# Performance work log

Measured on AMD Instinct MI355X. Metric: run time of the kernel, lower is better.

Reference implementation:

```python
import jax, jax.numpy as jnp
import numpy as np

N_NODES = 100000
N_EDGES = 1600000
D_IN = 128
D_HID = 128
D_OUT = 64


def setup_inputs() -> dict:
    key = jax.random.key(0)
    ks = jax.random.split(key, 8)
    x = jax.random.normal(ks[0], (N_NODES, D_IN), dtype=jnp.float32)
    edge_index = jax.random.randint(ks[1], (2, N_EDGES), 0, N_NODES, dtype=jnp.int64)
    s = 1.0 / np.sqrt(D_IN)
    W1l = jax.random.uniform(ks[2], (D_IN, D_HID), minval=-s, maxval=s, dtype=jnp.float32)
    W1r = jax.random.uniform(ks[3], (D_IN, D_HID), minval=-s, maxval=s, dtype=jnp.float32)
    b1 = jnp.zeros((D_HID,), dtype=jnp.float32)
    s2 = 1.0 / np.sqrt(D_HID)
    W2l = jax.random.uniform(ks[4], (D_HID, D_OUT), minval=-s2, maxval=s2, dtype=jnp.float32)
    W2r = jax.random.uniform(ks[5], (D_HID, D_OUT), minval=-s2, maxval=s2, dtype=jnp.float32)
    b2 = jnp.zeros((D_OUT,), dtype=jnp.float32)
    return {"x": x, "edge_index": edge_index, "drpt": 0,
            "W1l": W1l, "W1r": W1r, "b1": b1,
            "W2l": W2l, "W2r": W2r, "b2": b2}


def _mean_aggregate(x, src, dst, n_nodes):
    # gather source features along edges, scatter-mean to destinations
    gathered = x[src]                                   # [E, d]
    summed = jax.ops.segment_sum(gathered, dst, num_segments=n_nodes)  # [N, d]
    deg = jax.ops.segment_sum(jnp.ones((src.shape[0],), x.dtype), dst,
                              num_segments=n_nodes)     # [N]
    return summed / jnp.maximum(deg, 1.0)[:, None]


def _sage_conv(x, src, dst, Wl, Wr, b):
    # PyG SAGEConv (mean): out = agg @ Wl + b + x @ Wr
    agg = _mean_aggregate(x, src, dst, x.shape[0])
    return agg @ Wl + b + x @ Wr


def reference(x, edge_index, drpt, W1l, W1r, b1, W2l, W2r, b2):
    src, dst = edge_index[0], edge_index[1]
    h = _sage_conv(x, src, dst, W1l, W1r, b1)
    h = jax.nn.relu(h)
    # dropout is identity at inference (training=False)
    out = _sage_conv(h, src, dst, W2l, W2r, b2)
    return out
```

## Files before the change

kernel.cpp:

```cpp
#include <hip/hip_runtime.h>
#include <hip/hip_bf16.h>


#define N_NODES 100000
#define NGRP 6250
#define NBKT 391
#define ECHUNK 8192
#define BCAP 12288
#define NXB 12500
#define NWB 192

typedef __attribute__((ext_vector_type(8))) short short8v;
typedef __attribute__((ext_vector_type(4))) float f32x4;
typedef __attribute__((ext_vector_type(2))) uint u32x2;

__device__ inline ushort bf16_rne(float f) {
    union { float f; uint u; } c; c.f = f;
    uint u = c.u;
    return (ushort)((u + 0x7FFFu + ((u >> 16) & 1u)) >> 16);
}
__device__ inline float bf16_f(ushort h) {
    union { uint u; float f; } c; c.u = (uint)h << 16;
    return c.f;
}
__device__ inline unsigned char fp8_enc(float f) {
    union { float f; uint u; } c; c.f = f;
    uint u = c.u;
    uint s = (u >> 24) & 0x80u;
    uint a = u & 0x7FFFFFFFu;
    uint code;
    if (a >= 0x3C800000u) {
        uint r = a + 0x7FFFFu + ((a >> 20) & 1u);
        int e = (int)(r >> 23) - 120;
        uint mm = (r >> 20) & 7u;
        code = ((uint)e << 3) | mm;
        if (code > 0x7Eu) code = 0x7Eu;
    } else {
        code = (uint)(__uint_as_float(a) * 512.0f + 0.5f);
    }
    return (unsigned char)(s | code);
}

__device__ inline void gl_lds16(const void* g, void* l) {
    __builtin_amdgcn_global_load_lds(
        (const __attribute__((address_space(1))) uint*)g,
        (__attribute__((address_space(3))) uint*)l, 16, 0, 0);
}
__device__ inline uint lds_off(const void* p) {
    return (uint)(size_t)(const __attribute__((address_space(3))) char*)p;
}

__global__ __launch_bounds__(256) void k_prep(const float* __restrict__ x,
                                              const float* __restrict__ W1l,
                                              const float* __restrict__ W1r,
                                              const float* __restrict__ W2l,
                                              const float* __restrict__ W2r,
                                              const int* __restrict__ dst, int E,
                                              ushort* __restrict__ xh,
                                              unsigned char* __restrict__ xf8,
                                              ushort* __restrict__ BT1h,
                                              ushort* __restrict__ BT1l,
                                              ushort* __restrict__ BT2h,
                                              ushort* __restrict__ BT2l,
                                              int* __restrict__ bhist) {
    __shared__ int hsh[NBKT];
    const int b = blockIdx.x;
    if (b < NXB) {
        int i = (b * 256 + threadIdx.x) * 4;
        float4 v = *(const float4*)&x[i];
        ushort4 hh;
        hh.x = bf16_rne(v.x); hh.y = bf16_rne(v.y);
        hh.z = bf16_rne(v.z); hh.w = bf16_rne(v.w);
        *(ushort4*)&xh[i] = hh;
        uint f8 = (uint)fp8_enc(v.x) | ((uint)fp8_enc(v.y) << 8) |
                  ((uint)fp8_enc(v.z) << 16) | ((uint)fp8_enc(v.w) << 24);
        *(uint*)&xf8[i] = f8;
    } else if (b < NXB + NWB) {
        int id = (b - NXB) * 256 + threadIdx.x;
        if (id < 32768) {
            int n = id >> 8, k = id & 255;
            float v = (k < 128) ? W1l[k * 128 + n] : W1r[(k - 128) * 128 + n];
            ushort h = bf16_rne(v);
            BT1h[id] = h;
            BT1l[id] = bf16_rne(v - bf16_f(h));
        } else {
            int i = id - 32768;
            int n = i >> 7, k = i & 127;
            float v = (n < 64) ? W2l[k * 64 + n] : W2r[k * 64 + (n - 64)];
            ushort h = bf16_rne(v);
            BT2h[i] = h;
            BT2l[i] = bf16_rne(v - bf16_f(h));
        }
    } else {
        int bb = b - NXB - NWB;
        for (int i = threadIdx.x; i < NBKT; i += 256) hsh[i] = 0;
        __syncthreads();
        int b0 = bb * ECHUNK;
        for (int i = threadIdx.x; i < ECHUNK; i += 256) {
            int e = b0 + i;
            if (e < E) atomicAdd(&hsh[dst[e] >> 8], 1);
        }
        __syncthreads();
        for (int i = threadIdx.x; i < NBKT; i += 256)
            if (hsh[i]) atomicAdd(&bhist[i], hsh[i]);
    }
}

__global__ __launch_bounds__(512) void kA2_scan(const int* __restrict__ bhist,
                                                int* __restrict__ boff,
                                                int* __restrict__ bcur) {
    __shared__ int s[512];
    int t = threadIdx.x;
    s[t] = (t < NBKT) ? bhist[t] : 0;
    __syncthreads();
    for (int d = 1; d < 512; d <<= 1) {
        int v = (t >= d) ? s[t - d] : 0;
        __syncthreads();
        s[t] += v;
        __syncthreads();
    }
    if (t <= NBKT) {
        int e = (t == 0) ? 0 : s[t - 1];
        boff[t] = e;
        if (t < NBKT) bcur[t] = e;
    }
}

__global__ __launch_bounds__(256) void kA3_scatter(const int* __restrict__ src,
                                                   const int* __restrict__ dst,
                                                   int* __restrict__ bcur,
                                                   int* __restrict__ pairs, int E) {
    __shared__ int hist[NBKT];
    __shared__ int base[NBKT];
    __shared__ ushort rank[ECHUNK];
    for (int i = threadIdx.x; i < NBKT; i += 256) hist[i] = 0;
    __syncthreads();
    int b0 = blockIdx.x * ECHUNK;
    for (int i = threadIdx.x; i < ECHUNK; i += 256) {
        int e = b0 + i;
        if (e < E) rank[i] = (ushort)atomicAdd(&hist[dst[e] >> 8], 1);
    }
    __syncthreads();
    for (int i = threadIdx.x; i < NBKT; i += 256) {
        int c = hist[i];
        base[i] = c ? atomicAdd(&bcur[i], c) : 0;
    }
    __syncthreads();
    for (int i = threadIdx.x; i < ECHUNK; i += 256) {
        int e = b0 + i;
        if (e < E) {
            int d = dst[e];
            pairs[base[d >> 8] + rank[i]] = src[e] | ((d & 255) << 17);
        }
    }
}

__global__ __launch_bounds__(256) void kB_build(const int* __restrict__ pairs,
                                                const int* __restrict__ boff,
                                                int* __restrict__ csr,
                                                unsigned char* __restrict__ ldst,
                                                int* __restrict__ offsets,
                                                float* __restrict__ invdeg,
                                                int N, int E) {
    __shared__ int cnt[256];
    __shared__ int sc[256];
    __shared__ int cur[256];
    __shared__ int stage[BCAP];
    const int b = blockIdx.x;
    const int gbase = boff[b], gcount = boff[b + 1] - gbase;
    const int n0 = b << 8;
    const int t = threadIdx.x;

    cnt[t] = 0;
    __syncthreads();
    for (int i = t; i < gcount; i += 256)
        atomicAdd(&cnt[pairs[gbase + i] >> 17], 1);
    __syncthreads();
    sc[t] = cnt[t];
    __syncthreads();
    for (int d = 1; d < 256; d <<= 1) {
        int v = (t >= d) ? sc[t - d] : 0;
        __syncthreads();
        sc[t] += v;
        __syncthreads();
    }
    int excl = sc[t] - cnt[t];
    cur[t] = excl;
    int node = n0 + t;
    if (node < N) {
        offsets[node] = gbase + excl;
        invdeg[node] = 1.0f / fmaxf((float)cnt[t], 1.0f);
    }
    if (b == NBKT - 1 && t == 0) offsets[N] = E;
    __syncthreads();

    if (gcount <= BCAP) {
        for (int i = t; i < gcount; i += 256) {
            int p = pairs[gbase + i];
            int pos = atomicAdd(&cur[p >> 17], 1);
            stage[pos] = p;
        }
        __syncthreads();
        for (int i = t; i < gcount; i += 256) {
            int p = stage[i];
            csr[gbase + i] = p & 0x1FFFF;
            ldst[gbase + i] = (unsigned char)((p >> 17) & 15);
        }
    } else {
        for (int i = t; i < gcount; i += 256) {
            int p = pairs[gbase + i];
            int pos = atomicAdd(&cur[p >> 17], 1);
            csr[gbase + pos] = p & 0x1FFFF;
            ldst[gbase + pos] = (unsigned char)((p >> 17) & 15);
        }
    }
}

__global__ __launch_bounds__(256) void k_agg1(const unsigned char* __restrict__ xf8,
                                              const int* __restrict__ csr,
                                              const unsigned char* __restrict__ ldst,
                                              const int* __restrict__ off,
                                              const float* __restrict__ invdeg,
                                              ushort* __restrict__ ah, int E) {
    __shared__ char smem[32768];
    const int wv = threadIdx.x >> 6, lane = threadIdx.x & 63;
    const int g = blockIdx.x;
    const int gbase = off[g * 16], gend = off[g * 16 + 16];
    const int cnt = gend - gbase;
    const int m = lane & 15;
    const int e_meta = lane & 31;
    const int t_hi = lane >> 5;
    const int Emax = E - 1;
    char* stg = smem + wv * 4096;

    f32x4 acc[8] = {};
    const int nch = (cnt + 31) >> 5;

    int p0 = gbase + wv * 32;
    int se = csr[(p0 + e_meta < Emax) ? p0 + e_meta : Emax];
    int lb = (p0 + e_meta < gend) ? (int)ldst[p0 + e_meta] : 255;

    for (int ch = wv; ch < nch; ch += 4) {
        const char* rowbase = (const char*)xf8 + (size_t)se * 128;
        #pragma unroll
        for (int c = 0; c < 4; ++c)
            gl_lds16(rowbase + (c * 2 + t_hi) * 16, stg + c * 1024);

        asm volatile("s_waitcnt vmcnt(0)" ::: "memory");
        __builtin_amdgcn_sched_barrier(0);

        unsigned long long av = 0ull;
        #pragma unroll
        for (int j = 0; j < 8; ++j) {
            int k = (lane >> 4) * 8 + j;
            int b = __shfl(lb, k);
            av |= (b == m) ? (0x38ull << (8 * j)) : 0ull;
        }

        u32x2 tb[8];
        uint base0 = lds_off(stg) + lane * 8;
        #pragma unroll
        for (int t = 0; t < 8; ++t) {
            uint a1 = base0 + t * 512;
            asm volatile("ds_read_b64_tr_b8 %0, %1" : "=v"(tb[t]) : "v"(a1));
        }
        asm volatile("s_waitcnt lgkmcnt(0)" ::: "memory");
        __builtin_amdgcn_sched_barrier(0);
        #pragma unroll
        for (int t = 0; t < 8; ++t) {
            unsigned long long bv = ((unsigned long long)tb[t].y << 32) | tb[t].x;
            acc[t] = __builtin_amdgcn_mfma_f32_16x16x32_fp8_fp8(
                (long long)av, (long long)bv, acc[t], 0, 0, 0);
        }

        int p = gbase + (ch + 4) * 32;
        se = csr[(p + e_meta < Emax) ? p + e_meta : Emax];
        lb = (p + e_meta < gend) ? (int)ldst[p + e_meta] : 255;
    }

    __syncthreads();
    f32x4* red = (f32x4*)smem;
    #pragma unroll
    for (int t = 0; t < 8; ++t) red[(wv * 8 + t) * 64 + lane] = acc[t];
    __syncthreads();

    float idv[4];
    #pragma unroll
    for (int i = 0; i < 4; ++i) idv[i] = invdeg[g * 16 + (lane >> 4) * 4 + i];
    #pragma unroll
    for (int tt = 0; tt < 2; ++tt) {
        int t = wv * 2 + tt;
        f32x4 s = red[t * 64 + lane];
        s += red[(8 + t) * 64 + lane];
        s += red[(16 + t) * 64 + lane];
        s += red[(24 + t) * 64 + lane];
        #pragma unroll
        for (int i = 0; i < 4; ++i) {
            int node = g * 16 + (lane >> 4) * 4 + i;
            ah[(size_t)node * 128 + t * 16 + m] = bf16_rne(s[i] * idv[i]);
        }
    }
}

__global__ __launch_bounds__(256) void k_agg2(const ushort* __restrict__ hWl,
                                              const float* __restrict__ hWr,
                                              const int* __restrict__ csr,
                                              const unsigned char* __restrict__ ldst,
                                              const int* __restrict__ off,
                                              const float* __restrict__ invdeg,
                                              const float* __restrict__ b2,
                                              float* __restrict__ out, int E) {
    __shared__ char smem[16384];
    const int wv = threadIdx.x >> 6, lane = threadIdx.x & 63;
    const int g = blockIdx.x;
    const int gbase = off[g * 16], gend = off[g * 16 + 16];
    const int cnt = gend - gbase;
    const int m = lane & 15;
    const int phys = lane >> 3;
    const int E4 = (phys < 4) ? phys * 2 : (phys - 4) * 2 + 1;
    const int e_st = E4 * 4 + ((lane >> 1) & 3);
    const int e_meta = lane & 31;
    const int Emax = E - 1;
    char* stg = smem + wv * 4096;

    f32x4 acc[4] = {};
    const int nch = (cnt + 31) >> 5;

    int p0 = gbase + wv * 32;
    int se = csr[(p0 + e_st < Emax) ? p0 + e_st : Emax];
    int lb = (p0 + e_meta < gend) ? (int)ldst[p0 + e_meta] : 255;

    for (int ch = wv; ch < nch; ch += 4) {
        const char* gsrc = (const char*)hWl + (size_t)se * 128 + (lane & 1) * 16;
        #pragma unroll
        for (int c = 0; c < 4; ++c)
            gl_lds16(gsrc + c * 32, stg + c * 1024);

        asm volatile("s_waitcnt vmcnt(0)" ::: "memory");
        __builtin_amdgcn_sched_barrier(0);

        uint au[4];
        #pragma unroll
        for (int jp = 0; jp < 4; ++jp) {
            int k0 = (lane >> 4) * 8 + jp * 2;
            int b0 = __shfl(lb, k0);
            int b1 = __shfl(lb, k0 + 1);
            au[jp] = ((b0 == m) ? 0x3F80u : 0u) | (((b1 == m) ? 0x3F80u : 0u) << 16);
        }
        union { uint u[4]; short8v v; } A_;
        A_.u[0] = au[0]; A_.u[1] = au[1]; A_.u[2] = au[2]; A_.u[3] = au[3];

        u32x2 t1[4], t2[4];
        uint base0 = lds_off(stg) + lane * 8;
        #pragma unroll
        for (int t = 0; t < 4; ++t) {
            uint a1 = base0 + t * 1024;
            uint a2 = a1 + 512;
            asm volatile("ds_read_b64_tr_b16 %0, %1" : "=v"(t1[t]) : "v"(a1));
            asm volatile("ds_read_b64_tr_b16 %0, %1" : "=v"(t2[t]) : "v"(a2));
        }
        asm volatile("s_waitcnt lgkmcnt(0)" ::: "memory");
        __builtin_amdgcn_sched_barrier(0);
        #pragma unroll
        for (int t = 0; t < 4; ++t) {
            union { uint u[4]; short8v v; } B_;
            B_.u[0] = t1[t].x; B_.u[1] = t1[t].y;
            B_.u[2] = t2[t].x; B_.u[3] = t2[t].y;
            acc[t] = __builtin_amdgcn_mfma_f32_16x16x32_bf16(A_.v, B_.v, acc[t], 0, 0, 0);
        }

        int p = gbase + (ch + 4) * 32;
        se = csr[(p + e_st < Emax) ? p + e_st : Emax];
        lb = (p + e_meta < gend) ? (int)ldst[p + e_meta] : 255;
    }

    __syncthreads();
    f32x4* red = (f32x4*)smem;
    #pragma unroll
    for (int t = 0; t < 4; ++t) red[(wv * 4 + t) * 64 + lane] = acc[t];
    __syncthreads();

    float idv[4];
    #pragma unroll
    for (int i = 0; i < 4; ++i) idv[i] = invdeg[g * 16 + (lane >> 4) * 4 + i];
    {
        int t = wv;
        f32x4 s = red[t * 64 + lane];
        s += red[(4 + t) * 64 + lane];
        s += red[(8 + t) * 64 + lane];
        s += red[(12 + t) * 64 + lane];
        #pragma unroll
        for (int i = 0; i < 4; ++i) {
            int node = g * 16 + (lane >> 4) * 4 + i;
            size_t idx = (size_t)node * 64 + t * 16 + m;
            out[idx] = s[i] * idv[i] + hWr[idx] + b2[t * 16 + m];
        }
    }
}

__global__ __launch_bounds__(256) void k_mfma12(
    const ushort* __restrict__ Agg, const ushort* __restrict__ X,
    const ushort* __restrict__ B1h, const ushort* __restrict__ B1l,
    const ushort* __restrict__ B2h, const ushort* __restrict__ B2l,
    const float* __restrict__ b1,
    ushort* __restrict__ hWl, float* __restrict__ hWr, int M) {
    __shared__ ushort Ah[128 * 40], Bh[128 * 40], Bl[128 * 40];
    __shared__ ushort hT[4 * 128 * 40];

    const int tid = threadIdx.x;
    const int wid = tid >> 6, lane = tid & 63;
    const int wm = wid >> 1, wn = wid & 1;
    const int m0 = blockIdx.x * 128;
    const int rl = lane & 15, kof = (lane >> 4) * 8;
    const int rq = lane >> 4;

    f32x4 acc[4][4] = {};
    for (int kc = 0; kc < 8; ++kc) {
        #pragma unroll
        for (int r = 0; r < 2; ++r) {
            int chunk = tid + 256 * r;
            int row = chunk >> 2, cq = chunk & 3;
            int gk = kc * 32 + cq * 8;
            int ldso = row * 40 + cq * 8;
            int grow = m0 + row;
            if (grow >= M) grow = M - 1;
            if (gk >= 128) {
                *(short8v*)&Ah[ldso] = *(const short8v*)&X[(size_t)grow * 128 + gk - 128];
            } else {
                *(short8v*)&Ah[ldso] = *(const short8v*)&Agg[(size_t)grow * 128 + gk];
            }
            *(short8v*)&Bh[ldso] = *(const short8v*)&B1h[row * 256 + gk];
            *(short8v*)&Bl[ldso] = *(const short8v*)&B1l[row * 256 + gk];
        }
        __syncthreads();

        short8v a_h[4], b_h[4], b_l[4];
        #pragma unroll
        for (int f = 0; f < 4; ++f) {
            int ra = wm * 64 + f * 16 + rl;
            int rb = wn * 64 + f * 16 + rl;
            a_h[f] = *(const short8v*)&Ah[ra * 40 + kof];
            b_h[f] = *(const short8v*)&Bh[rb * 40 + kof];
            b_l[f] = *(const short8v*)&Bl[rb * 40 + kof];
        }
        #pragma unroll
        for (int mf = 0; mf < 4; ++mf)
            #pragma unroll
            for (int nf = 0; nf < 4; ++nf) {
                acc[mf][nf] = __builtin_amdgcn_mfma_f32_16x16x32_bf16(a_h[mf], b_h[nf], acc[mf][nf], 0, 0, 0);
                acc[mf][nf] = __builtin_amdgcn_mfma_f32_16x16x32_bf16(a_h[mf], b_l[nf], acc[mf][nf], 0, 0, 0);
            }
        __syncthreads();
    }

    #pragma unroll
    for (int mf = 0; mf < 4; ++mf)
        #pragma unroll
        for (int nf = 0; nf < 4; ++nf) {
            int col = wn * 64 + nf * 16 + rl;
            float bv = b1[col];
            #pragma unroll
            for (int i = 0; i < 4; ++i) {
                int rloc = wm * 64 + mf * 16 + rq * 4 + i;
                float v = fmaxf(acc[mf][nf][i] + bv, 0.0f);
                hT[((col >> 5) * 128 + rloc) * 40 + (col & 31)] = bf16_rne(v);
            }
        }
    __syncthreads();

    f32x4 acc2[4][4] = {};
    for (int kc = 0; kc < 4; ++kc) {
        #pragma unroll
        for (int r = 0; r < 2; ++r) {
            int chunk = tid + 256 * r;
            int row = chunk >> 2, cq = chunk & 3;
            int gk = kc * 32 + cq * 8;
            int ldso = row * 40 + cq * 8;
            *(short8v*)&Bh[ldso] = *(const short8v*)&B2h[row * 128 + gk];
            *(short8v*)&Bl[ldso] = *(const short8v*)&B2l[row * 128 + gk];
        }
        __syncthreads();

        short8v a_h[4], b_h[4], b_l[4];
        #pragma unroll
        for (int f = 0; f < 4; ++f) {
            int ra = wm * 64 + f * 16 + rl;
            int rb = wn * 64 + f * 16 + rl;
            a_h[f] = *(const short8v*)&hT[(kc * 128 + ra) * 40 + kof];
            b_h[f] = *(const short8v*)&Bh[rb * 40 + kof];
            b_l[f] = *(const short8v*)&Bl[rb * 40 + kof];
        }
        #pragma unroll
        for (int mf = 0; mf < 4; ++mf)
            #pragma unroll
            for (int nf = 0; nf < 4; ++nf) {
                acc2[mf][nf] = __builtin_amdgcn_mfma_f32_16x16x32_bf16(a_h[mf], b_h[nf], acc2[mf][nf], 0, 0, 0);
                acc2[mf][nf] = __builtin_amdgcn_mfma_f32_16x16x32_bf16(a_h[mf], b_l[nf], acc2[mf][nf], 0, 0, 0);
            }
        __syncthreads();
    }

    #pragma unroll
    for (int mf = 0; mf < 4; ++mf)
        #pragma unroll
        for (int nf = 0; nf < 4; ++nf) {
            int col = wn * 64 + nf * 16 + rl;
            #pragma unroll
            for (int i = 0; i < 4; ++i) {
                int row = m0 + wm * 64 + mf * 16 + rq * 4 + i;
                if (row < M) {
                    float v = acc2[mf][nf][i];
                    if (col < 64) hWl[(size_t)row * 64 + col] = bf16_rne(v);
                    else          hWr[(size_t)row * 64 + col - 64] = v;
                }
            }
        }
}

extern "C" void kernel_launch(void* const* d_in, const int* in_sizes, int n_in,
                              void* d_out, int out_size, void* d_ws, size_t ws_size,
                              hipStream_t stream) {
    const float* x   = (const float*)d_in[0];
    const int*   ei  = (const int*)d_in[1];
    const float* W1l = (const float*)d_in[3];
    const float* W1r = (const float*)d_in[4];
    const float* b1  = (const float*)d_in[5];
    const float* W2l = (const float*)d_in[6];
    const float* W2r = (const float*)d_in[7];
    const float* b2  = (const float*)d_in[8];
    float* out = (float*)d_out;

    const int N = N_NODES;
    const int E = in_sizes[1] / 2;
    const int* src = ei;
    const int* dst = ei + E;
    const int NEB = (E + ECHUNK - 1) / ECHUNK;

    char* ws = (char*)d_ws;
    int*           bhist   = (int*)   (ws + 0);
    int*           boff    = (int*)   (ws + 4096);
    int*           bcur    = (int*)   (ws + 8192);
    int*           offsets = (int*)   (ws + 12288);
    float*         invdeg  = (float*) (ws + 417792);
    int*           csr     = (int*)   (ws + 819200);
    unsigned char* ldst    = (unsigned char*)(ws + 7220224);
    unsigned char* x_f8    = (unsigned char*)(ws + 8821760);
    ushort*        x_hi    = (ushort*)(ws + 21622784);
    ushort*        agg_hi  = (ushort*)(ws + 47223808);
    float*         hWr     = (float*) (ws + 98425856);
    ushort*        BT1h    = (ushort*)(ws + 124026880);
    ushort*        BT1l    = (ushort*)(ws + 124092416);
    ushort*        BT2h    = (ushort*)(ws + 124157952);
    ushort*        BT2l    = (ushort*)(ws + 124190720);
    int*           pairs   = (int*)   (ws + 98425856);
    ushort*        hWl     = (ushort*)(ws + 72824832);

    hipMemsetAsync(bhist, 0, NBKT * 4, stream);

    k_prep<<<NXB + NWB + NEB, 256, 0, stream>>>(x, W1l, W1r, W2l, W2r, dst, E,
                                                x_hi, x_f8, BT1h, BT1l, BT2h, BT2l, bhist);
    kA2_scan<<<1, 512, 0, stream>>>(bhist, boff, bcur);
    kA3_scatter<<<NEB, 256, 0, stream>>>(src, dst, bcur, pairs, E);
    kB_build<<<NBKT, 256, 0, stream>>>(pairs, boff, csr, ldst, offsets, invdeg, N, E);

    k_agg1<<<NGRP, 256, 0, stream>>>(x_f8, csr, ldst, offsets, invdeg, agg_hi, E);

    const int MB = (N + 127) / 128;
    k_mfma12<<<MB, 256, 0, stream>>>(agg_hi, x_hi, BT1h, BT1l, BT2h, BT2l,
                                     b1, hWl, hWr, N);

    k_agg2<<<NGRP, 256, 0, stream>>>(hWl, hWr, csr, ldst, offsets, invdeg, b2, out, E);
}
```

Measured before the change: 198.5 us.

## Assign one wavefront per node group in aggregation kernels, drop LDS reduction

Both aggregation kernels now give each wavefront its own 16-node group instead of splitting a group's edge chunks across four waves. This removes the cross-wave LDS reduction and the two __syncthreads, halves k_agg1's shared memory, and adds a launch-bounds occupancy hint of 8. The next chunk's index loads are issued right after the current chunk's global-to-LDS copies, and the transposed LDS reads are split into two halves to cut register pressure. The cost is a longer serial edge loop per wave and more load imbalance when groups have uneven degree.

```diff
diff --git a/kernel.cpp b/kernel.cpp
--- a/kernel.cpp
+++ b/kernel.cpp
@@ -216,15 +216,16 @@
     }
 }
 
-__global__ __launch_bounds__(256) void k_agg1(const unsigned char* __restrict__ xf8,
-                                              const int* __restrict__ csr,
-                                              const unsigned char* __restrict__ ldst,
-                                              const int* __restrict__ off,
-                                              const float* __restrict__ invdeg,
-                                              ushort* __restrict__ ah, int E) {
-    __shared__ char smem[32768];
+__global__ __launch_bounds__(256, 8) void k_agg1(const unsigned char* __restrict__ xf8,
+                                                 const int* __restrict__ csr,
+                                                 const unsigned char* __restrict__ ldst,
+                                                 const int* __restrict__ off,
+                                                 const float* __restrict__ invdeg,
+                                                 ushort* __restrict__ ah, int E) {
+    __shared__ char smem[16384];
     const int wv = threadIdx.x >> 6, lane = threadIdx.x & 63;
-    const int g = blockIdx.x;
+    const int g = blockIdx.x * 4 + wv;
+    if (g >= NGRP) return;
     const int gbase = off[g * 16], gend = off[g * 16 + 16];
     const int cnt = gend - gbase;
     const int m = lane & 15;
@@ -236,15 +237,19 @@
     f32x4 acc[8] = {};
     const int nch = (cnt + 31) >> 5;
 
-    int p0 = gbase + wv * 32;
-    int se = csr[(p0 + e_meta < Emax) ? p0 + e_meta : Emax];
-    int lb = (p0 + e_meta < gend) ? (int)ldst[p0 + e_meta] : 255;
-
-    for (int ch = wv; ch < nch; ch += 4) {
+    int pe = gbase + e_meta;
+    int se = csr[(pe < Emax) ? pe : Emax];
+    int lb = (pe < gend) ? (int)ldst[pe] : 255;
+
+    for (int ch = 0; ch < nch; ++ch) {
         const char* rowbase = (const char*)xf8 + (size_t)se * 128;
         #pragma unroll
         for (int c = 0; c < 4; ++c)
             gl_lds16(rowbase + (c * 2 + t_hi) * 16, stg + c * 1024);
+
+        int p = gbase + (ch + 1) * 32 + e_meta;
+        se = csr[(p < Emax) ? p : Emax];
+        int lbn = (p < gend) ? (int)ldst[p] : 255;
 
         asm volatile("s_waitcnt vmcnt(0)" ::: "memory");
         __builtin_amdgcn_sched_barrier(0);
@@ -257,62 +262,53 @@
             av |= (b == m) ? (0x38ull << (8 * j)) : 0ull;
         }
 
-        u32x2 tb[8];
         uint base0 = lds_off(stg) + lane * 8;
         #pragma unroll
-        for (int t = 0; t < 8; ++t) {
-            uint a1 = base0 + t * 512;
-            asm volatile("ds_read_b64_tr_b8 %0, %1" : "=v"(tb[t]) : "v"(a1));
-        }
-        asm volatile("s_waitcnt lgkmcnt(0)" ::: "memory");
-        __builtin_amdgcn_sched_barrier(0);
-        #pragma unroll
-        for (int t = 0; t < 8; ++t) {
-            unsigned long long bv = ((unsigned long long)tb[t].y << 32) | tb[t].x;
-            acc[t] = __builtin_amdgcn_mfma_f32_16x16x32_fp8_fp8(
-                (long long)av, (long long)bv, acc[t], 0, 0, 0);
-        }
-
-        int p = gbase + (ch + 4) * 32;
-        se = csr[(p + e_meta < Emax) ? p + e_meta : Emax];
-        lb = (p + e_meta < gend) ? (int)ldst[p + e_meta] : 255;
-    }
-
-    __syncthreads();
-    f32x4* red = (f32x4*)smem;
-    #pragma unroll
-    for (int t = 0; t < 8; ++t) red[(wv * 8 + t) * 64 + lane] = acc[t];
-    __syncthreads();
+        for (int th = 0; th < 2; ++th) {
+            u32x2 tb[4];
+            #pragma unroll
+            for (int t = 0; t < 4; ++t) {
+                uint a1 = base0 + (th * 4 + t) * 512;
+                asm volatile("ds_read_b64_tr_b8 %0, %1" : "=v"(tb[t]) : "v"(a1));
+            }
+            asm volatile("s_waitcnt lgkmcnt(0)" ::: "memory");
+            __builtin_amdgcn_sched_barrier(0);
+            #pragma unroll
+            for (int t = 0; t < 4; ++t) {
+                unsigned long long bv = ((unsigned long long)tb[t].y << 32) | tb[t].x;
+                acc[th * 4 + t] = __builtin_amdgcn_mfma_f32_16x16x32_fp8_fp8(
+                    (long long)av, (long long)bv, acc[th * 4 + t], 0, 0, 0);
+            }
+            __builtin_amdgcn_sched_barrier(0);
+        }
+        lb = lbn;
+    }
 
     float idv[4];
     #pragma unroll
     for (int i = 0; i < 4; ++i) idv[i] = invdeg[g * 16 + (lane >> 4) * 4 + i];
     #pragma unroll
-    for (int tt = 0; tt < 2; ++tt) {
-        int t = wv * 2 + tt;
-        f32x4 s = red[t * 64 + lane];
-        s += red[(8 + t) * 64 + lane];
-        s += red[(16 + t) * 64 + lane];
-        s += red[(24 + t) * 64 + lane];
+    for (int t = 0; t < 8; ++t) {
         #pragma unroll
         for (int i = 0; i < 4; ++i) {
             int node = g * 16 + (lane >> 4) * 4 + i;
-            ah[(size_t)node * 128 + t * 16 + m] = bf16_rne(s[i] * idv[i]);
-        }
-    }
-}
-
-__global__ __launch_bounds__(256) void k_agg2(const ushort* __restrict__ hWl,
-                                              const float* __restrict__ hWr,
-                                              const int* __restrict__ csr,
-                                              const unsigned char* __restrict__ ldst,
-                                              const int* __restrict__ off,
-                                              const float* __restrict__ invdeg,
-                                              const float* __restrict__ b2,
-                                              float* __restrict__ out, int E) {
+            ah[(size_t)node * 128 + t * 16 + m] = bf16_rne(acc[t][i] * idv[i]);
+        }
+    }
+}
+
+__global__ __launch_bounds__(256, 8) void k_agg2(const ushort* __restrict__ hWl,
+                                                 const float* __restrict__ hWr,
+                                                 const int* __restrict__ csr,
+                                                 const unsigned char* __restrict__ ldst,
+                                                 const int* __restrict__ off,
+                                                 const float* __restrict__ invdeg,
+                                                 const float* __restrict__ b2,
+                                                 float* __restrict__ out, int E) {
     __shared__ char smem[16384];
     const int wv = threadIdx.x >> 6, lane = threadIdx.x & 63;
-    const int g = blockIdx.x;
+    const int g = blockIdx.x * 4 + wv;
+    if (g >= NGRP) return;
     const int gbase = off[g * 16], gend = off[g * 16 + 16];
     const int cnt = gend - gbase;
     const int m = lane & 15;
@@ -326,15 +322,22 @@
     f32x4 acc[4] = {};
     const int nch = (cnt + 31) >> 5;
 
-    int p0 = gbase + wv * 32;
-    int se = csr[(p0 + e_st < Emax) ? p0 + e_st : Emax];
-    int lb = (p0 + e_meta < gend) ? (int)ldst[p0 + e_meta] : 255;
-
-    for (int ch = wv; ch < nch; ch += 4) {
+    int ps = gbase + e_st;
+    int se = csr[(ps < Emax) ? ps : Emax];
+    int pm = gbase + e_meta;
+    int lb = (pm < gend) ? (int)ldst[pm] : 255;
+
+    for (int ch = 0; ch < nch; ++ch) {
         const char* gsrc = (const char*)hWl + (size_t)se * 128 + (lane & 1) * 16;
         #pragma unroll
         for (int c = 0; c < 4; ++c)
             gl_lds16(gsrc + c * 32, stg + c * 1024);
+
+        int p = gbase + (ch + 1) * 32;
+        int ps2 = p + e_st;
+        se = csr[(ps2 < Emax) ? ps2 : Emax];
+        int pm2 = p + e_meta;
+        int lbn = (pm2 < gend) ? (int)ldst[pm2] : 255;
 
         asm volatile("s_waitcnt vmcnt(0)" ::: "memory");
         __builtin_amdgcn_sched_barrier(0);
@@ -350,50 +353,42 @@
         union { uint u[4]; short8v v; } A_;
         A_.u[0] = au[0]; A_.u[1] = au[1]; A_.u[2] = au[2]; A_.u[3] = au[3];
 
-        u32x2 t1[4], t2[4];
         uint base0 = lds_off(stg) + lane * 8;
         #pragma unroll
-        for (int t = 0; t < 4; ++t) {
-            uint a1 = base0 + t * 1024;
-            uint a2 = a1 + 512;
-            asm volatile("ds_read_b64_tr_b16 %0, %1" : "=v"(t1[t]) : "v"(a1));
-            asm volatile("ds_read_b64_tr_b16 %0, %1" : "=v"(t2[t]) : "v"(a2));
-        }
-        asm volatile("s_waitcnt lgkmcnt(0)" ::: "memory");
-        __builtin_amdgcn_sched_barrier(0);
-        #pragma unroll
-        for (int t = 0; t < 4; ++t) {
-            union { uint u[4]; short8v v; } B_;
-            B_.u[0] = t1[t].x; B_.u[1] = t1[t].y;
-            B_.u[2] = t2[t].x; B_.u[3] = t2[t].y;
-            acc[t] = __builtin_amdgcn_mfma_f32_16x16x32_bf16(A_.v, B_.v, acc[t], 0, 0, 0);
-        }
-
-        int p = gbase + (ch + 4) * 32;
-        se = csr[(p + e_st < Emax) ? p + e_st : Emax];
-        lb = (p + e_meta < gend) ? (int)ldst[p + e_meta] : 255;
-    }
-
-    __syncthreads();
-    f32x4* red = (f32x4*)smem;
-    #pragma unroll
-    for (int t = 0; t < 4; ++t) red[(wv * 4 + t) * 64 + lane] = acc[t];
-    __syncthreads();
+        for (int th = 0; th < 2; ++th) {
+            u32x2 t1[2], t2[2];
+            #pragma unroll
+            for (int t = 0; t < 2; ++t) {
+                uint a1 = base0 + (th * 2 + t) * 1024;
+                uint a2 = a1 + 512;
+                asm volatile("ds_read_b64_tr_b16 %0, %1" : "=v"(t1[t]) : "v"(a1));
+                asm volatile("ds_read_b64_tr_b16 %0, %1" : "=v"(t2[t]) : "v"(a2));
+            }
+            asm volatile("s_waitcnt lgkmcnt(0)" ::: "memory");
+            __builtin_amdgcn_sched_barrier(0);
+            #pragma unroll
+            for (int t = 0; t < 2; ++t) {
+                union { uint u[4]; short8v v; } B_;
+                B_.u[0] = t1[t].x; B_.u[1] = t1[t].y;
+                B_.u[2] = t2[t].x; B_.u[3] = t2[t].y;
+                acc[th * 2 + t] = __builtin_amdgcn_mfma_f32_16x16x32_bf16(
+                    A_.v, B_.v, acc[th * 2 + t], 0, 0, 0);
+            }
+            __builtin_amdgcn_sched_barrier(0);
+        }
+        lb = lbn;
+    }
 
     float idv[4];
     #pragma unroll
     for (int i = 0; i < 4; ++i) idv[i] = invdeg[g * 16 + (lane >> 4) * 4 + i];
-    {
-        int t = wv;
-        f32x4 s = red[t * 64 + lane];
-        s += red[(4 + t) * 64 + lane];
-        s += red[(8 + t) * 64 + lane];
-        s += red[(12 + t) * 64 + lane];
+    #pragma unroll
+    for (int t = 0; t < 4; ++t) {
         #pragma unroll
         for (int i = 0; i < 4; ++i) {
             int node = g * 16 + (lane >> 4) * 4 + i;
             size_t idx = (size_t)node * 64 + t * 16 + m;
-            out[idx] = s[i] * idv[i] + hWr[idx] + b2[t * 16 + m];
+            out[idx] = acc[t][i] * idv[i] + hWr[idx] + b2[t * 16 + m];
         }
     }
 }
@@ -563,11 +558,12 @@
     kA3_scatter<<<NEB, 256, 0, stream>>>(src, dst, bcur, pairs, E);
     kB_build<<<NBKT, 256, 0, stream>>>(pairs, boff, csr, ldst, offsets, invdeg, N, E);
 
-    k_agg1<<<NGRP, 256, 0, stream>>>(x_f8, csr, ldst, offsets, invdeg, agg_hi, E);
+    const int GAGG = (NGRP + 3) / 4;
+    k_agg1<<<GAGG, 256, 0, stream>>>(x_f8, csr, ldst, offsets, invdeg, agg_hi, E);
 
     const int MB = (N + 127) / 128;
     k_mfma12<<<MB, 256, 0, stream>>>(agg_hi, x_hi, BT1h, BT1l, BT2h, BT2l,
                                      b1, hWl, hWr, N);
 
-    k_agg2<<<NGRP, 256, 0, stream>>>(hWl, hWr, csr, ldst, offsets, invdeg, b2, out, E);
-}
+    k_agg2<<<GAGG, 256, 0, stream>>>(hWl, hWr, csr, ldst, offsets, invdeg, b2, out, E);
+}
```

Result: no change. 198.2 us (-0.1%).
